# Optimization experiments

Measured on AMD Instinct MI355X. Metric: run time of the kernel, lower is better.

Reference implementation:

```python
import jax, jax.numpy as jnp
import numpy as np

NBR_SIZE = 3
ALPHA = -1.0
EPS = 1e-12  # torch F.normalize eps


def _l2norm(x, axis):
    n = jnp.sqrt(jnp.sum(x * x, axis=axis, keepdims=True))
    return x / jnp.maximum(n, EPS)


def setup_inputs() -> dict:
    key = jax.random.key(0)
    k1, k2 = jax.random.split(key)
    nbrs = jax.random.normal(k1, (4, 4, 64, 128, 128), dtype=jnp.float32)  # [b, n_frames, c, h, w]
    ref = jax.random.normal(k2, (4, 64, 128, 128), dtype=jnp.float32)      # [b, c, h, w]
    return {"nbrs": nbrs, "ref": ref}


def reference(nbrs, ref):
    b, n, c, h, w = nbrs.shape
    pad = NBR_SIZE // 2
    # mean over neighbor frames, detached in the original
    mean = jax.lax.stop_gradient(jnp.mean(nbrs, axis=1))          # [b,c,h,w]
    # ref is detached+cloned before normalization in the original
    ref_n = _l2norm(jax.lax.stop_gradient(ref), axis=1)           # [b,c,h,w], unit-norm over c

    outs = []
    for i in range(n):  # small fixed number of frames
        nbr = nbrs[:, i]                                          # [b,c,h,w]
        wdiff = jnp.exp(ALPHA * (nbr - mean) ** 2)                # [b,c,h,w]
        p = jnp.pad(nbr, ((0, 0), (0, 0), (pad, pad), (pad, pad)), mode='reflect')
        # unfold: k2 = NBR_SIZE**2 shifted views -> [b,c,k2,h,w]
        win = jnp.stack([p[:, :, dy:dy + h, dx:dx + w]
                         for dy in range(NBR_SIZE) for dx in range(NBR_SIZE)], axis=2)
        win_n = _l2norm(win, axis=1)                              # normalize over channels
        # per-pixel cosine similarity: [b,k2,h,w]
        d = jnp.einsum('bchw,bckhw->bkhw', ref_n, win_n)
        wt = jax.nn.softmax(d, axis=1)                            # softmax over k2 window positions
        # aggregate normalized window features: [b,c,h,w]
        agg = jnp.einsum('bkhw,bckhw->bchw', wt, win_n)
        outs.append(agg * wdiff)

    return jnp.stack(outs + [ref], axis=1)                        # [b, n+1, c, h, w]
```

## Files before the change

kernel.cpp:

```cpp
#include <hip/hip_runtime.h>
#include <math.h>

namespace {

constexpr int B_ = 4, N_ = 4, C_ = 64, H_ = 128, W_ = 128;
constexpr int HW_ = H_ * W_;
constexpr int CPB = 4;
constexpr int NWIN = C_ / CPB;

__global__ __launch_bounds__(256) void copyref_kernel(const float* __restrict__ ref,
                                                      float* __restrict__ out) {
    int t = blockIdx.x * 256 + threadIdx.x;
    int f = t * 4;
    int b = f / (C_ * HW_);
    int within = f - b * (C_ * HW_);
    float4 v = *reinterpret_cast<const float4*>(ref + (size_t)b * C_ * HW_ + within);
    *reinterpret_cast<float4*>(out + (size_t)(b * 5 + N_) * C_ * HW_ + within) = v;
}

__global__ __launch_bounds__(256) void localcorr_kernel(const float* __restrict__ nbrs,
                                                        const float* __restrict__ ref,
                                                        float* __restrict__ out) {
    __shared__ float s_own[2 * CPB][4][128];
    __shared__ float s_nrm[4][128];

    const int blk = blockIdx.x;
    const int ypair = blk & 63;
    const int bi = blk >> 6;
    const int i = bi & 3;
    const int b = bi >> 2;
    const int t = (int)threadIdx.x;
    const int x = t & 127;
    const int ry = t >> 7;
    const int y0 = ypair * 2;
    const int y = y0 + ry;

    const int xm = (x == 0) ? 1 : x - 1;
    const int xp = (x == W_ - 1) ? W_ - 2 : x + 1;
    const int gyA = (y0 == 0) ? 1 : y0 - 1;
    const int gyC = y0 + 1;
    const int gyD = (y0 + 2 == H_) ? H_ - 2 : y0 + 2;
    const int myRowA = (ry == 0) ? gyA : gyC;
    const int myRowB = (ry == 0) ? y0 : gyD;

    const float* __restrict__ nb = nbrs + (size_t)(b * N_ + i) * C_ * HW_;
    const float* __restrict__ rp = ref + (size_t)b * C_ * HW_;
    const int offA = myRowA * W_ + x;
    const int offB = myRowB * W_ + x;
    const int offR = y * W_ + x;

    float dot[9];
#pragma unroll
    for (int k = 0; k < 9; ++k) dot[k] = 0.f;
    float nA = 0.f, nB = 0.f, r2 = 0.f;

    float co0[CPB], co1[CPB], crf[CPB];
    float no0[CPB], no1[CPB], nrf[CPB];
#pragma unroll
    for (int u = 0; u < CPB; ++u) {
        const size_t co = (size_t)u * HW_;
        co0[u] = nb[co + offA]; co1[u] = nb[co + offB]; crf[u] = rp[co + offR];
    }
#pragma unroll 1
    for (int w = 0; w < NWIN; ++w) {
        const int base = (w & 1) * CPB;
#pragma unroll
        for (int u = 0; u < CPB; ++u) {
            s_own[base + u][2 * ry + 0][x] = co0[u];
            s_own[base + u][2 * ry + 1][x] = co1[u];
        }
        __syncthreads();
        if (w + 1 < NWIN) {
#pragma unroll
            for (int u = 0; u < CPB; ++u) {
                const size_t co = (size_t)((w + 1) * CPB + u) * HW_;
                no0[u] = nb[co + offA]; no1[u] = nb[co + offB]; nrf[u] = rp[co + offR];
            }
        }
#pragma unroll
        for (int u = 0; u < CPB; ++u) {
            const float w00 = s_own[base + u][ry + 0][xm], w02 = s_own[base + u][ry + 0][xp];
            const float w10 = s_own[base + u][ry + 1][xm], w12 = s_own[base + u][ry + 1][xp];
            const float w20 = s_own[base + u][ry + 2][xm], w22 = s_own[base + u][ry + 2][xp];
            float w01, w11, w21;
            if (ry == 0) { w01 = co0[u]; w11 = co1[u]; w21 = s_own[base + u][2][x]; }
            else         { w01 = s_own[base + u][1][x]; w11 = co0[u]; w21 = co1[u]; }
            const float rf = crf[u];
            nA += co0[u] * co0[u]; nB += co1[u] * co1[u]; r2 += rf * rf;
            dot[0] += rf * w00; dot[1] += rf * w01; dot[2] += rf * w02;
            dot[3] += rf * w10; dot[4] += rf * w11; dot[5] += rf * w12;
            dot[6] += rf * w20; dot[7] += rf * w21; dot[8] += rf * w22;
        }
#pragma unroll
        for (int u = 0; u < CPB; ++u) { co0[u] = no0[u]; co1[u] = no1[u]; crf[u] = nrf[u]; }
    }

    s_nrm[2 * ry + 0][x] = nA;
    s_nrm[2 * ry + 1][x] = nB;
    __syncthreads();
    float nk[9];
    nk[0] = s_nrm[ry + 0][xm]; nk[1] = s_nrm[ry + 0][x]; nk[2] = s_nrm[ry + 0][xp];
    nk[3] = s_nrm[ry + 1][xm]; nk[4] = s_nrm[ry + 1][x]; nk[5] = s_nrm[ry + 1][xp];
    nk[6] = s_nrm[ry + 2][xm]; nk[7] = s_nrm[ry + 2][x]; nk[8] = s_nrm[ry + 2][xp];

    const float invr = rsqrtf(fmaxf(r2, 1e-24f));
    float inv[9], d[9];
#pragma unroll
    for (int k = 0; k < 9; ++k) {
        inv[k] = rsqrtf(fmaxf(nk[k], 1e-24f));
        d[k] = dot[k] * invr * inv[k];
    }
    float mx = d[0];
#pragma unroll
    for (int k = 1; k < 9; ++k) mx = fmaxf(mx, d[k]);
    float ssum = 0.f;
#pragma unroll
    for (int k = 0; k < 9; ++k) { d[k] = __expf(d[k] - mx); ssum += d[k]; }
    const float is = 1.f / ssum;
    float wtp[9];
#pragma unroll
    for (int k = 0; k < 9; ++k) wtp[k] = d[k] * is * inv[k];

    const float* __restrict__ pm0 = nbrs + (size_t)(b * N_ + ((i + 1) & 3)) * C_ * HW_;
    const float* __restrict__ pm1 = nbrs + (size_t)(b * N_ + ((i + 2) & 3)) * C_ * HW_;
    const float* __restrict__ pm2 = nbrs + (size_t)(b * N_ + ((i + 3) & 3)) * C_ * HW_;
    float* __restrict__ op = out + (size_t)(b * 5 + i) * C_ * HW_ + offR;

    float q0c[CPB], q1c[CPB], q2c[CPB];
    float q0n[CPB], q1n[CPB], q2n[CPB];
#pragma unroll
    for (int u = 0; u < CPB; ++u) {
        const size_t co = (size_t)u * HW_;
        co0[u] = nb[co + offA]; co1[u] = nb[co + offB];
        q0c[u] = pm0[co + offR]; q1c[u] = pm1[co + offR]; q2c[u] = pm2[co + offR];
    }
#pragma unroll 1
    for (int w = 0; w < NWIN; ++w) {
        const int base = (w & 1) * CPB;
#pragma unroll
        for (int u = 0; u < CPB; ++u) {
            s_own[base + u][2 * ry + 0][x] = co0[u];
            s_own[base + u][2 * ry + 1][x] = co1[u];
        }
        __syncthreads();
        if (w + 1 < NWIN) {
#pragma unroll
            for (int u = 0; u < CPB; ++u) {
                const size_t co = (size_t)((w + 1) * CPB + u) * HW_;
                no0[u] = nb[co + offA]; no1[u] = nb[co + offB];
                q0n[u] = pm0[co + offR]; q1n[u] = pm1[co + offR]; q2n[u] = pm2[co + offR];
            }
        }
#pragma unroll
        for (int u = 0; u < CPB; ++u) {
            const float w00 = s_own[base + u][ry + 0][xm], w02 = s_own[base + u][ry + 0][xp];
            const float w10 = s_own[base + u][ry + 1][xm], w12 = s_own[base + u][ry + 1][xp];
            const float w20 = s_own[base + u][ry + 2][xm], w22 = s_own[base + u][ry + 2][xp];
            float w01, w11, w21;
            if (ry == 0) { w01 = co0[u]; w11 = co1[u]; w21 = s_own[base + u][2][x]; }
            else         { w01 = s_own[base + u][1][x]; w11 = co0[u]; w21 = co1[u]; }
            const float agg = wtp[0] * w00 + wtp[1] * w01 + wtp[2] * w02
                            + wtp[3] * w10 + wtp[4] * w11 + wtp[5] * w12
                            + wtp[6] * w20 + wtp[7] * w21 + wtp[8] * w22;
            const float ctr = w11;
            const float dd = ctr - 0.25f * (ctr + q0c[u] + q1c[u] + q2c[u]);
            op[(size_t)(w * CPB + u) * HW_] = agg * __expf(-dd * dd);
        }
#pragma unroll
        for (int u = 0; u < CPB; ++u) {
            co0[u] = no0[u]; co1[u] = no1[u];
            q0c[u] = q0n[u]; q1c[u] = q1n[u]; q2c[u] = q2n[u];
        }
    }
}

}

extern "C" void kernel_launch(void* const* d_in, const int* in_sizes, int n_in,
                              void* d_out, int out_size, void* d_ws, size_t ws_size,
                              hipStream_t stream) {
    const float* nbrs = (const float*)d_in[0];
    const float* ref = (const float*)d_in[1];
    float* out = (float*)d_out;

    copyref_kernel<<<(B_ * C_ * HW_ / 4) / 256, 256, 0, stream>>>(ref, out);

    localcorr_kernel<<<B_ * N_ * (H_ / 2), 256, 0, stream>>>(nbrs, ref, out);
}
```

Before: 74.84 us.

## Tile four rows per block with two pixels per thread and float2 loads

Each block now covers 4 output rows instead of 2, and each thread handles two adjacent x pixels using float2 loads and stores. Halo rows are loaded by the first 128 threads and stored in a 6-row shared buffer. This cuts halo re-reads of neighbour rows from 2x to 1.5x and halves the number of memory instructions. In exchange the grid shrinks to 512 blocks, some threads sit idle during halo loads, and register pressure goes up from the two 9-element accumulator sets.

After: 67.31 us. 10.1% less time.

```diff
diff --git a/kernel.cpp b/kernel.cpp
--- a/kernel.cpp
+++ b/kernel.cpp
@@ -7,6 +7,7 @@
 constexpr int HW_ = H_ * W_;
 constexpr int CPB = 4;
 constexpr int NWIN = C_ / CPB;
+constexpr int ROWS = 4;
 
 __global__ __launch_bounds__(256) void copyref_kernel(const float* __restrict__ ref,
                                                       float* __restrict__ out) {
@@ -18,157 +19,212 @@
     *reinterpret_cast<float4*>(out + (size_t)(b * 5 + N_) * C_ * HW_ + within) = v;
 }
 
+__device__ __forceinline__ float2 ld2(const float* p) {
+    return *reinterpret_cast<const float2*>(p);
+}
+
 __global__ __launch_bounds__(256) void localcorr_kernel(const float* __restrict__ nbrs,
                                                         const float* __restrict__ ref,
                                                         float* __restrict__ out) {
-    __shared__ float s_own[2 * CPB][4][128];
-    __shared__ float s_nrm[4][128];
+    __shared__ float2 s_own[2 * CPB][6][64];
+    __shared__ float2 s_nrm[6][64];
 
     const int blk = blockIdx.x;
-    const int ypair = blk & 63;
-    const int bi = blk >> 6;
+    const int ytile = blk & 31;
+    const int bi = blk >> 5;
     const int i = bi & 3;
     const int b = bi >> 2;
     const int t = (int)threadIdx.x;
-    const int x = t & 127;
-    const int ry = t >> 7;
-    const int y0 = ypair * 2;
+    const int xh = t & 63;
+    const int ry = t >> 6;
+    const int x0 = xh * 2;
+    const int y0 = ytile * ROWS;
     const int y = y0 + ry;
 
-    const int xm = (x == 0) ? 1 : x - 1;
-    const int xp = (x == W_ - 1) ? W_ - 2 : x + 1;
-    const int gyA = (y0 == 0) ? 1 : y0 - 1;
-    const int gyC = y0 + 1;
-    const int gyD = (y0 + 2 == H_) ? H_ - 2 : y0 + 2;
-    const int myRowA = (ry == 0) ? gyA : gyC;
-    const int myRowB = (ry == 0) ? y0 : gyD;
+    const int xlh = (xh == 0) ? 0 : xh - 1;
+    const int xrh = (xh == 63) ? 63 : xh + 1;
+    const int gTop = (y0 == 0) ? 1 : y0 - 1;
+    const int gBot = (y0 + ROWS == H_) ? H_ - 2 : y0 + ROWS;
+
+    const bool isHalo = (t < 128);
+    const int haloRow = (t < 64) ? 0 : 5;
+    const int haloOff = ((t < 64) ? gTop : gBot) * W_ + x0;
 
     const float* __restrict__ nb = nbrs + (size_t)(b * N_ + i) * C_ * HW_;
     const float* __restrict__ rp = ref + (size_t)b * C_ * HW_;
-    const int offA = myRowA * W_ + x;
-    const int offB = myRowB * W_ + x;
-    const int offR = y * W_ + x;
-
-    float dot[9];
-#pragma unroll
-    for (int k = 0; k < 9; ++k) dot[k] = 0.f;
-    float nA = 0.f, nB = 0.f, r2 = 0.f;
-
-    float co0[CPB], co1[CPB], crf[CPB];
-    float no0[CPB], no1[CPB], nrf[CPB];
+    const int offO = y * W_ + x0;
+
+    float d0[9], d1[9];
+#pragma unroll
+    for (int k = 0; k < 9; ++k) { d0[k] = 0.f; d1[k] = 0.f; }
+    float na = 0.f, nb2 = 0.f, r20 = 0.f, r21 = 0.f, hna = 0.f, hnb = 0.f;
+
+    float2 cO[CPB], cR[CPB], cH[CPB];
+    float2 nO[CPB], nR[CPB], nH[CPB];
 #pragma unroll
     for (int u = 0; u < CPB; ++u) {
         const size_t co = (size_t)u * HW_;
-        co0[u] = nb[co + offA]; co1[u] = nb[co + offB]; crf[u] = rp[co + offR];
+        cO[u] = ld2(nb + co + offO);
+        cR[u] = ld2(rp + co + offO);
+        cH[u] = isHalo ? ld2(nb + co + haloOff) : make_float2(0.f, 0.f);
+        nH[u] = make_float2(0.f, 0.f);
     }
 #pragma unroll 1
     for (int w = 0; w < NWIN; ++w) {
         const int base = (w & 1) * CPB;
 #pragma unroll
         for (int u = 0; u < CPB; ++u) {
-            s_own[base + u][2 * ry + 0][x] = co0[u];
-            s_own[base + u][2 * ry + 1][x] = co1[u];
+            s_own[base + u][ry + 1][xh] = cO[u];
+            if (isHalo) s_own[base + u][haloRow][xh] = cH[u];
         }
         __syncthreads();
         if (w + 1 < NWIN) {
 #pragma unroll
             for (int u = 0; u < CPB; ++u) {
                 const size_t co = (size_t)((w + 1) * CPB + u) * HW_;
-                no0[u] = nb[co + offA]; no1[u] = nb[co + offB]; nrf[u] = rp[co + offR];
-            }
-        }
-#pragma unroll
-        for (int u = 0; u < CPB; ++u) {
-            const float w00 = s_own[base + u][ry + 0][xm], w02 = s_own[base + u][ry + 0][xp];
-            const float w10 = s_own[base + u][ry + 1][xm], w12 = s_own[base + u][ry + 1][xp];
-            const float w20 = s_own[base + u][ry + 2][xm], w22 = s_own[base + u][ry + 2][xp];
-            float w01, w11, w21;
-            if (ry == 0) { w01 = co0[u]; w11 = co1[u]; w21 = s_own[base + u][2][x]; }
-            else         { w01 = s_own[base + u][1][x]; w11 = co0[u]; w21 = co1[u]; }
-            const float rf = crf[u];
-            nA += co0[u] * co0[u]; nB += co1[u] * co1[u]; r2 += rf * rf;
-            dot[0] += rf * w00; dot[1] += rf * w01; dot[2] += rf * w02;
-            dot[3] += rf * w10; dot[4] += rf * w11; dot[5] += rf * w12;
-            dot[6] += rf * w20; dot[7] += rf * w21; dot[8] += rf * w22;
-        }
-#pragma unroll
-        for (int u = 0; u < CPB; ++u) { co0[u] = no0[u]; co1[u] = no1[u]; crf[u] = nrf[u]; }
-    }
-
-    s_nrm[2 * ry + 0][x] = nA;
-    s_nrm[2 * ry + 1][x] = nB;
+                nO[u] = ld2(nb + co + offO);
+                nR[u] = ld2(rp + co + offO);
+                if (isHalo) nH[u] = ld2(nb + co + haloOff);
+            }
+        }
+#pragma unroll
+        for (int u = 0; u < CPB; ++u) {
+            const float2 rf = cR[u];
+            r20 += rf.x * rf.x; r21 += rf.y * rf.y;
+            na += cO[u].x * cO[u].x; nb2 += cO[u].y * cO[u].y;
+            if (isHalo) { hna += cH[u].x * cH[u].x; hnb += cH[u].y * cH[u].y; }
+#pragma unroll
+            for (int wr = 0; wr < 3; ++wr) {
+                const int r = ry + wr;
+                const float2 Lp = s_own[base + u][r][xlh];
+                const float2 Cp = (wr == 1) ? cO[u] : s_own[base + u][r][xh];
+                const float2 Rp = s_own[base + u][r][xrh];
+                d0[3 * wr + 0] += rf.x * Lp.y;
+                d0[3 * wr + 1] += rf.x * Cp.x;
+                d0[3 * wr + 2] += rf.x * Cp.y;
+                d1[3 * wr + 0] += rf.y * Cp.x;
+                d1[3 * wr + 1] += rf.y * Cp.y;
+                d1[3 * wr + 2] += rf.y * Rp.x;
+            }
+        }
+#pragma unroll
+        for (int u = 0; u < CPB; ++u) { cO[u] = nO[u]; cR[u] = nR[u]; cH[u] = nH[u]; }
+    }
+
+    s_nrm[ry + 1][xh] = make_float2(na, nb2);
+    if (isHalo) s_nrm[haloRow][xh] = make_float2(hna, hnb);
     __syncthreads();
-    float nk[9];
-    nk[0] = s_nrm[ry + 0][xm]; nk[1] = s_nrm[ry + 0][x]; nk[2] = s_nrm[ry + 0][xp];
-    nk[3] = s_nrm[ry + 1][xm]; nk[4] = s_nrm[ry + 1][x]; nk[5] = s_nrm[ry + 1][xp];
-    nk[6] = s_nrm[ry + 2][xm]; nk[7] = s_nrm[ry + 2][x]; nk[8] = s_nrm[ry + 2][xp];
-
-    const float invr = rsqrtf(fmaxf(r2, 1e-24f));
-    float inv[9], d[9];
-#pragma unroll
-    for (int k = 0; k < 9; ++k) {
-        inv[k] = rsqrtf(fmaxf(nk[k], 1e-24f));
-        d[k] = dot[k] * invr * inv[k];
-    }
-    float mx = d[0];
-#pragma unroll
-    for (int k = 1; k < 9; ++k) mx = fmaxf(mx, d[k]);
-    float ssum = 0.f;
-#pragma unroll
-    for (int k = 0; k < 9; ++k) { d[k] = __expf(d[k] - mx); ssum += d[k]; }
-    const float is = 1.f / ssum;
-    float wtp[9];
-#pragma unroll
-    for (int k = 0; k < 9; ++k) wtp[k] = d[k] * is * inv[k];
+
+    float nk0[9], nk1[9];
+#pragma unroll
+    for (int wr = 0; wr < 3; ++wr) {
+        const int r = ry + wr;
+        const float2 Lp = s_nrm[r][xlh];
+        const float2 Cp = (wr == 1) ? make_float2(na, nb2) : s_nrm[r][xh];
+        const float2 Rp = s_nrm[r][xrh];
+        nk0[3 * wr + 0] = Lp.y; nk0[3 * wr + 1] = Cp.x; nk0[3 * wr + 2] = Cp.y;
+        nk1[3 * wr + 0] = Cp.x; nk1[3 * wr + 1] = Cp.y; nk1[3 * wr + 2] = Rp.x;
+    }
+
+    float w0[9], w1[9];
+    {
+        const float invr = rsqrtf(fmaxf(r20, 1e-24f));
+        float iv[9], dd[9];
+#pragma unroll
+        for (int k = 0; k < 9; ++k) {
+            iv[k] = rsqrtf(fmaxf(nk0[k], 1e-24f));
+            dd[k] = d0[k] * invr * iv[k];
+        }
+        float mx = dd[0];
+#pragma unroll
+        for (int k = 1; k < 9; ++k) mx = fmaxf(mx, dd[k]);
+        float ss = 0.f;
+#pragma unroll
+        for (int k = 0; k < 9; ++k) { dd[k] = __expf(dd[k] - mx); ss += dd[k]; }
+        const float is = 1.f / ss;
+#pragma unroll
+        for (int k = 0; k < 9; ++k) w0[k] = dd[k] * is * iv[k];
+    }
+    {
+        const float invr = rsqrtf(fmaxf(r21, 1e-24f));
+        float iv[9], dd[9];
+#pragma unroll
+        for (int k = 0; k < 9; ++k) {
+            iv[k] = rsqrtf(fmaxf(nk1[k], 1e-24f));
+            dd[k] = d1[k] * invr * iv[k];
+        }
+        float mx = dd[0];
+#pragma unroll
+        for (int k = 1; k < 9; ++k) mx = fmaxf(mx, dd[k]);
+        float ss = 0.f;
+#pragma unroll
+        for (int k = 0; k < 9; ++k) { dd[k] = __expf(dd[k] - mx); ss += dd[k]; }
+        const float is = 1.f / ss;
+#pragma unroll
+        for (int k = 0; k < 9; ++k) w1[k] = dd[k] * is * iv[k];
+    }
 
     const float* __restrict__ pm0 = nbrs + (size_t)(b * N_ + ((i + 1) & 3)) * C_ * HW_;
     const float* __restrict__ pm1 = nbrs + (size_t)(b * N_ + ((i + 2) & 3)) * C_ * HW_;
     const float* __restrict__ pm2 = nbrs + (size_t)(b * N_ + ((i + 3) & 3)) * C_ * HW_;
-    float* __restrict__ op = out + (size_t)(b * 5 + i) * C_ * HW_ + offR;
-
-    float q0c[CPB], q1c[CPB], q2c[CPB];
-    float q0n[CPB], q1n[CPB], q2n[CPB];
+    float* __restrict__ op = out + (size_t)(b * 5 + i) * C_ * HW_ + offO;
+
+    float2 q0c[CPB], q1c[CPB], q2c[CPB];
+    float2 q0n[CPB], q1n[CPB], q2n[CPB];
 #pragma unroll
     for (int u = 0; u < CPB; ++u) {
         const size_t co = (size_t)u * HW_;
-        co0[u] = nb[co + offA]; co1[u] = nb[co + offB];
-        q0c[u] = pm0[co + offR]; q1c[u] = pm1[co + offR]; q2c[u] = pm2[co + offR];
+        cO[u] = ld2(nb + co + offO);
+        cH[u] = isHalo ? ld2(nb + co + haloOff) : make_float2(0.f, 0.f);
+        q0c[u] = ld2(pm0 + co + offO);
+        q1c[u] = ld2(pm1 + co + offO);
+        q2c[u] = ld2(pm2 + co + offO);
     }
 #pragma unroll 1
     for (int w = 0; w < NWIN; ++w) {
         const int base = (w & 1) * CPB;
 #pragma unroll
         for (int u = 0; u < CPB; ++u) {
-            s_own[base + u][2 * ry + 0][x] = co0[u];
-            s_own[base + u][2 * ry + 1][x] = co1[u];
+            s_own[base + u][ry + 1][xh] = cO[u];
+            if (isHalo) s_own[base + u][haloRow][xh] = cH[u];
         }
         __syncthreads();
         if (w + 1 < NWIN) {
 #pragma unroll
             for (int u = 0; u < CPB; ++u) {
                 const size_t co = (size_t)((w + 1) * CPB + u) * HW_;
-                no0[u] = nb[co + offA]; no1[u] = nb[co + offB];
-                q0n[u] = pm0[co + offR]; q1n[u] = pm1[co + offR]; q2n[u] = pm2[co + offR];
-            }
-        }
-#pragma unroll
-        for (int u = 0; u < CPB; ++u) {
-            const float w00 = s_own[base + u][ry + 0][xm], w02 = s_own[base + u][ry + 0][xp];
-            const float w10 = s_own[base + u][ry + 1][xm], w12 = s_own[base + u][ry + 1][xp];
-            const float w20 = s_own[base + u][ry + 2][xm], w22 = s_own[base + u][ry + 2][xp];
-            float w01, w11, w21;
-            if (ry == 0) { w01 = co0[u]; w11 = co1[u]; w21 = s_own[base + u][2][x]; }
-            else         { w01 = s_own[base + u][1][x]; w11 = co0[u]; w21 = co1[u]; }
-            const float agg = wtp[0] * w00 + wtp[1] * w01 + wtp[2] * w02
-                            + wtp[3] * w10 + wtp[4] * w11 + wtp[5] * w12
-                            + wtp[6] * w20 + wtp[7] * w21 + wtp[8] * w22;
-            const float ctr = w11;
-            const float dd = ctr - 0.25f * (ctr + q0c[u] + q1c[u] + q2c[u]);
-            op[(size_t)(w * CPB + u) * HW_] = agg * __expf(-dd * dd);
-        }
-#pragma unroll
-        for (int u = 0; u < CPB; ++u) {
-            co0[u] = no0[u]; co1[u] = no1[u];
+                nO[u] = ld2(nb + co + offO);
+                if (isHalo) nH[u] = ld2(nb + co + haloOff);
+                q0n[u] = ld2(pm0 + co + offO);
+                q1n[u] = ld2(pm1 + co + offO);
+                q2n[u] = ld2(pm2 + co + offO);
+            }
+        }
+#pragma unroll
+        for (int u = 0; u < CPB; ++u) {
+            float agg0 = 0.f, agg1 = 0.f;
+#pragma unroll
+            for (int wr = 0; wr < 3; ++wr) {
+                const int r = ry + wr;
+                const float2 Lp = s_own[base + u][r][xlh];
+                const float2 Cp = (wr == 1) ? cO[u] : s_own[base + u][r][xh];
+                const float2 Rp = s_own[base + u][r][xrh];
+                agg0 += w0[3 * wr + 0] * Lp.y + w0[3 * wr + 1] * Cp.x + w0[3 * wr + 2] * Cp.y;
+                agg1 += w1[3 * wr + 0] * Cp.x + w1[3 * wr + 1] * Cp.y + w1[3 * wr + 2] * Rp.x;
+            }
+            const float2 ctr = cO[u];
+            const float s0 = ctr.x + q0c[u].x + q1c[u].x + q2c[u].x;
+            const float s1 = ctr.y + q0c[u].y + q1c[u].y + q2c[u].y;
+            const float dd0 = ctr.x - 0.25f * s0;
+            const float dd1 = ctr.y - 0.25f * s1;
+            float2 o2;
+            o2.x = agg0 * __expf(-dd0 * dd0);
+            o2.y = agg1 * __expf(-dd1 * dd1);
+            *reinterpret_cast<float2*>(op + (size_t)(w * CPB + u) * HW_) = o2;
+        }
+#pragma unroll
+        for (int u = 0; u < CPB; ++u) {
+            cO[u] = nO[u]; cH[u] = nH[u];
             q0c[u] = q0n[u]; q1c[u] = q1n[u]; q2c[u] = q2n[u];
         }
     }
@@ -185,5 +241,5 @@
 
     copyref_kernel<<<(B_ * C_ * HW_ / 4) / 256, 256, 0, stream>>>(ref, out);
 
-    localcorr_kernel<<<B_ * N_ * (H_ / 2), 256, 0, stream>>>(nbrs, ref, out);
-}
+    localcorr_kernel<<<B_ * N_ * (H_ / ROWS), 256, 0, stream>>>(nbrs, ref, out);
+}
```

## Process all four neighbor frames per block to share ref and mean loads

Applied to the files above, without the earlier changes.

Each block now handles one (batch, row-pair) tile for all four frames instead of one frame, so the grid shrinks from 1024 to 256 blocks. The reference channel values are loaded once and reused across frames. The frame mean comes from the center values already in registers, so the three extra neighbor-frame loads in the second pass go away. In exchange, register and shared-memory use per thread grow sharply, and with only one block per CU there is much less parallelism to hide memory latency.

After: 165.7 us. +121.5%, slower.

```diff
diff --git a/kernel.cpp b/kernel.cpp
--- a/kernel.cpp
+++ b/kernel.cpp
@@ -21,14 +21,12 @@
 __global__ __launch_bounds__(256) void localcorr_kernel(const float* __restrict__ nbrs,
                                                         const float* __restrict__ ref,
                                                         float* __restrict__ out) {
-    __shared__ float s_own[2 * CPB][4][128];
-    __shared__ float s_nrm[4][128];
+    __shared__ float s_win[2][CPB][4][4][128];
+    __shared__ float s_nrm[4][4][128];
 
     const int blk = blockIdx.x;
     const int ypair = blk & 63;
-    const int bi = blk >> 6;
-    const int i = bi & 3;
-    const int b = bi >> 2;
+    const int b = blk >> 6;
     const int t = (int)threadIdx.x;
     const int x = t & 127;
     const int ry = t >> 7;
@@ -43,134 +41,183 @@
     const int myRowA = (ry == 0) ? gyA : gyC;
     const int myRowB = (ry == 0) ? y0 : gyD;
 
-    const float* __restrict__ nb = nbrs + (size_t)(b * N_ + i) * C_ * HW_;
+    const float* __restrict__ nbq[4];
+#pragma unroll
+    for (int j = 0; j < 4; ++j) nbq[j] = nbrs + (size_t)(b * N_ + j) * C_ * HW_;
     const float* __restrict__ rp = ref + (size_t)b * C_ * HW_;
     const int offA = myRowA * W_ + x;
     const int offB = myRowB * W_ + x;
     const int offR = y * W_ + x;
 
-    float dot[9];
-#pragma unroll
-    for (int k = 0; k < 9; ++k) dot[k] = 0.f;
-    float nA = 0.f, nB = 0.f, r2 = 0.f;
-
-    float co0[CPB], co1[CPB], crf[CPB];
-    float no0[CPB], no1[CPB], nrf[CPB];
+    float dot[4][9];
+#pragma unroll
+    for (int j = 0; j < 4; ++j)
+#pragma unroll
+        for (int k = 0; k < 9; ++k) dot[j][k] = 0.f;
+    float nA[4], nB[4];
+#pragma unroll
+    for (int j = 0; j < 4; ++j) { nA[j] = 0.f; nB[j] = 0.f; }
+    float r2 = 0.f;
+
+    float c0[CPB][4], c1[CPB][4], crf[CPB];
+    float n0[CPB][4], n1[CPB][4], nrf[CPB];
 #pragma unroll
     for (int u = 0; u < CPB; ++u) {
         const size_t co = (size_t)u * HW_;
-        co0[u] = nb[co + offA]; co1[u] = nb[co + offB]; crf[u] = rp[co + offR];
+#pragma unroll
+        for (int j = 0; j < 4; ++j) {
+            c0[u][j] = nbq[j][co + offA];
+            c1[u][j] = nbq[j][co + offB];
+        }
+        crf[u] = rp[co + offR];
     }
 #pragma unroll 1
     for (int w = 0; w < NWIN; ++w) {
-        const int base = (w & 1) * CPB;
-#pragma unroll
-        for (int u = 0; u < CPB; ++u) {
-            s_own[base + u][2 * ry + 0][x] = co0[u];
-            s_own[base + u][2 * ry + 1][x] = co1[u];
-        }
+        const int buf = w & 1;
+#pragma unroll
+        for (int u = 0; u < CPB; ++u)
+#pragma unroll
+            for (int j = 0; j < 4; ++j) {
+                s_win[buf][u][j][2 * ry + 0][x] = c0[u][j];
+                s_win[buf][u][j][2 * ry + 1][x] = c1[u][j];
+            }
         __syncthreads();
         if (w + 1 < NWIN) {
 #pragma unroll
             for (int u = 0; u < CPB; ++u) {
                 const size_t co = (size_t)((w + 1) * CPB + u) * HW_;
-                no0[u] = nb[co + offA]; no1[u] = nb[co + offB]; nrf[u] = rp[co + offR];
+#pragma unroll
+                for (int j = 0; j < 4; ++j) {
+                    n0[u][j] = nbq[j][co + offA];
+                    n1[u][j] = nbq[j][co + offB];
+                }
+                nrf[u] = rp[co + offR];
             }
         }
 #pragma unroll
         for (int u = 0; u < CPB; ++u) {
-            const float w00 = s_own[base + u][ry + 0][xm], w02 = s_own[base + u][ry + 0][xp];
-            const float w10 = s_own[base + u][ry + 1][xm], w12 = s_own[base + u][ry + 1][xp];
-            const float w20 = s_own[base + u][ry + 2][xm], w22 = s_own[base + u][ry + 2][xp];
-            float w01, w11, w21;
-            if (ry == 0) { w01 = co0[u]; w11 = co1[u]; w21 = s_own[base + u][2][x]; }
-            else         { w01 = s_own[base + u][1][x]; w11 = co0[u]; w21 = co1[u]; }
             const float rf = crf[u];
-            nA += co0[u] * co0[u]; nB += co1[u] * co1[u]; r2 += rf * rf;
-            dot[0] += rf * w00; dot[1] += rf * w01; dot[2] += rf * w02;
-            dot[3] += rf * w10; dot[4] += rf * w11; dot[5] += rf * w12;
-            dot[6] += rf * w20; dot[7] += rf * w21; dot[8] += rf * w22;
-        }
-#pragma unroll
-        for (int u = 0; u < CPB; ++u) { co0[u] = no0[u]; co1[u] = no1[u]; crf[u] = nrf[u]; }
-    }
-
-    s_nrm[2 * ry + 0][x] = nA;
-    s_nrm[2 * ry + 1][x] = nB;
+            r2 += rf * rf;
+#pragma unroll
+            for (int j = 0; j < 4; ++j) {
+                const float* sc = &s_win[buf][u][j][0][0];
+                const float w00 = sc[(ry + 0) * 128 + xm], w02 = sc[(ry + 0) * 128 + xp];
+                const float w10 = sc[(ry + 1) * 128 + xm], w12 = sc[(ry + 1) * 128 + xp];
+                const float w20 = sc[(ry + 2) * 128 + xm], w22 = sc[(ry + 2) * 128 + xp];
+                float w01, w11, w21;
+                if (ry == 0) { w01 = c0[u][j]; w11 = c1[u][j]; w21 = sc[2 * 128 + x]; }
+                else         { w01 = sc[1 * 128 + x]; w11 = c0[u][j]; w21 = c1[u][j]; }
+                nA[j] += c0[u][j] * c0[u][j];
+                nB[j] += c1[u][j] * c1[u][j];
+                dot[j][0] += rf * w00; dot[j][1] += rf * w01; dot[j][2] += rf * w02;
+                dot[j][3] += rf * w10; dot[j][4] += rf * w11; dot[j][5] += rf * w12;
+                dot[j][6] += rf * w20; dot[j][7] += rf * w21; dot[j][8] += rf * w22;
+            }
+        }
+#pragma unroll
+        for (int u = 0; u < CPB; ++u) {
+#pragma unroll
+            for (int j = 0; j < 4; ++j) { c0[u][j] = n0[u][j]; c1[u][j] = n1[u][j]; }
+            crf[u] = nrf[u];
+        }
+    }
+
+#pragma unroll
+    for (int j = 0; j < 4; ++j) {
+        s_nrm[j][2 * ry + 0][x] = nA[j];
+        s_nrm[j][2 * ry + 1][x] = nB[j];
+    }
     __syncthreads();
-    float nk[9];
-    nk[0] = s_nrm[ry + 0][xm]; nk[1] = s_nrm[ry + 0][x]; nk[2] = s_nrm[ry + 0][xp];
-    nk[3] = s_nrm[ry + 1][xm]; nk[4] = s_nrm[ry + 1][x]; nk[5] = s_nrm[ry + 1][xp];
-    nk[6] = s_nrm[ry + 2][xm]; nk[7] = s_nrm[ry + 2][x]; nk[8] = s_nrm[ry + 2][xp];
 
     const float invr = rsqrtf(fmaxf(r2, 1e-24f));
-    float inv[9], d[9];
-#pragma unroll
-    for (int k = 0; k < 9; ++k) {
-        inv[k] = rsqrtf(fmaxf(nk[k], 1e-24f));
-        d[k] = dot[k] * invr * inv[k];
-    }
-    float mx = d[0];
-#pragma unroll
-    for (int k = 1; k < 9; ++k) mx = fmaxf(mx, d[k]);
-    float ssum = 0.f;
-#pragma unroll
-    for (int k = 0; k < 9; ++k) { d[k] = __expf(d[k] - mx); ssum += d[k]; }
-    const float is = 1.f / ssum;
-    float wtp[9];
-#pragma unroll
-    for (int k = 0; k < 9; ++k) wtp[k] = d[k] * is * inv[k];
-
-    const float* __restrict__ pm0 = nbrs + (size_t)(b * N_ + ((i + 1) & 3)) * C_ * HW_;
-    const float* __restrict__ pm1 = nbrs + (size_t)(b * N_ + ((i + 2) & 3)) * C_ * HW_;
-    const float* __restrict__ pm2 = nbrs + (size_t)(b * N_ + ((i + 3) & 3)) * C_ * HW_;
-    float* __restrict__ op = out + (size_t)(b * 5 + i) * C_ * HW_ + offR;
-
-    float q0c[CPB], q1c[CPB], q2c[CPB];
-    float q0n[CPB], q1n[CPB], q2n[CPB];
+    float wtp[4][9];
+#pragma unroll
+    for (int j = 0; j < 4; ++j) {
+        float nk[9];
+        nk[0] = s_nrm[j][ry + 0][xm]; nk[1] = s_nrm[j][ry + 0][x]; nk[2] = s_nrm[j][ry + 0][xp];
+        nk[3] = s_nrm[j][ry + 1][xm]; nk[4] = s_nrm[j][ry + 1][x]; nk[5] = s_nrm[j][ry + 1][xp];
+        nk[6] = s_nrm[j][ry + 2][xm]; nk[7] = s_nrm[j][ry + 2][x]; nk[8] = s_nrm[j][ry + 2][xp];
+        float iv[9], d[9];
+#pragma unroll
+        for (int k = 0; k < 9; ++k) {
+            iv[k] = rsqrtf(fmaxf(nk[k], 1e-24f));
+            d[k] = dot[j][k] * invr * iv[k];
+        }
+        float mx = d[0];
+#pragma unroll
+        for (int k = 1; k < 9; ++k) mx = fmaxf(mx, d[k]);
+        float ss = 0.f;
+#pragma unroll
+        for (int k = 0; k < 9; ++k) { d[k] = __expf(d[k] - mx); ss += d[k]; }
+        const float is = 1.f / ss;
+#pragma unroll
+        for (int k = 0; k < 9; ++k) wtp[j][k] = d[k] * is * iv[k];
+    }
+
+    float* __restrict__ op[4];
+#pragma unroll
+    for (int j = 0; j < 4; ++j) op[j] = out + (size_t)(b * 5 + j) * C_ * HW_ + offR;
+
 #pragma unroll
     for (int u = 0; u < CPB; ++u) {
         const size_t co = (size_t)u * HW_;
-        co0[u] = nb[co + offA]; co1[u] = nb[co + offB];
-        q0c[u] = pm0[co + offR]; q1c[u] = pm1[co + offR]; q2c[u] = pm2[co + offR];
+#pragma unroll
+        for (int j = 0; j < 4; ++j) {
+            c0[u][j] = nbq[j][co + offA];
+            c1[u][j] = nbq[j][co + offB];
+        }
     }
 #pragma unroll 1
     for (int w = 0; w < NWIN; ++w) {
-        const int base = (w & 1) * CPB;
-#pragma unroll
-        for (int u = 0; u < CPB; ++u) {
-            s_own[base + u][2 * ry + 0][x] = co0[u];
-            s_own[base + u][2 * ry + 1][x] = co1[u];
-        }
+        const int buf = w & 1;
+#pragma unroll
+        for (int u = 0; u < CPB; ++u)
+#pragma unroll
+            for (int j = 0; j < 4; ++j) {
+                s_win[buf][u][j][2 * ry + 0][x] = c0[u][j];
+                s_win[buf][u][j][2 * ry + 1][x] = c1[u][j];
+            }
         __syncthreads();
         if (w + 1 < NWIN) {
 #pragma unroll
             for (int u = 0; u < CPB; ++u) {
                 const size_t co = (size_t)((w + 1) * CPB + u) * HW_;
-                no0[u] = nb[co + offA]; no1[u] = nb[co + offB];
-                q0n[u] = pm0[co + offR]; q1n[u] = pm1[co + offR]; q2n[u] = pm2[co + offR];
+#pragma unroll
+                for (int j = 0; j < 4; ++j) {
+                    n0[u][j] = nbq[j][co + offA];
+                    n1[u][j] = nbq[j][co + offB];
+                }
             }
         }
 #pragma unroll
         for (int u = 0; u < CPB; ++u) {
-            const float w00 = s_own[base + u][ry + 0][xm], w02 = s_own[base + u][ry + 0][xp];
-            const float w10 = s_own[base + u][ry + 1][xm], w12 = s_own[base + u][ry + 1][xp];
-            const float w20 = s_own[base + u][ry + 2][xm], w22 = s_own[base + u][ry + 2][xp];
-            float w01, w11, w21;
-            if (ry == 0) { w01 = co0[u]; w11 = co1[u]; w21 = s_own[base + u][2][x]; }
-            else         { w01 = s_own[base + u][1][x]; w11 = co0[u]; w21 = co1[u]; }
-            const float agg = wtp[0] * w00 + wtp[1] * w01 + wtp[2] * w02
-                            + wtp[3] * w10 + wtp[4] * w11 + wtp[5] * w12
-                            + wtp[6] * w20 + wtp[7] * w21 + wtp[8] * w22;
-            const float ctr = w11;
-            const float dd = ctr - 0.25f * (ctr + q0c[u] + q1c[u] + q2c[u]);
-            op[(size_t)(w * CPB + u) * HW_] = agg * __expf(-dd * dd);
-        }
-#pragma unroll
-        for (int u = 0; u < CPB; ++u) {
-            co0[u] = no0[u]; co1[u] = no1[u];
-            q0c[u] = q0n[u]; q1c[u] = q1n[u]; q2c[u] = q2n[u];
-        }
+            float agg[4], ctr[4];
+#pragma unroll
+            for (int j = 0; j < 4; ++j) {
+                const float* sc = &s_win[buf][u][j][0][0];
+                const float w00 = sc[(ry + 0) * 128 + xm], w02 = sc[(ry + 0) * 128 + xp];
+                const float w10 = sc[(ry + 1) * 128 + xm], w12 = sc[(ry + 1) * 128 + xp];
+                const float w20 = sc[(ry + 2) * 128 + xm], w22 = sc[(ry + 2) * 128 + xp];
+                float w01, w11, w21;
+                if (ry == 0) { w01 = c0[u][j]; w11 = c1[u][j]; w21 = sc[2 * 128 + x]; }
+                else         { w01 = sc[1 * 128 + x]; w11 = c0[u][j]; w21 = c1[u][j]; }
+                agg[j] = wtp[j][0] * w00 + wtp[j][1] * w01 + wtp[j][2] * w02
+                       + wtp[j][3] * w10 + wtp[j][4] * w11 + wtp[j][5] * w12
+                       + wtp[j][6] * w20 + wtp[j][7] * w21 + wtp[j][8] * w22;
+                ctr[j] = w11;
+            }
+            const float mu = 0.25f * (ctr[0] + ctr[1] + ctr[2] + ctr[3]);
+            const size_t co = (size_t)(w * CPB + u) * HW_;
+#pragma unroll
+            for (int j = 0; j < 4; ++j) {
+                const float dd = ctr[j] - mu;
+                op[j][co] = agg[j] * __expf(-dd * dd);
+            }
+        }
+#pragma unroll
+        for (int u = 0; u < CPB; ++u)
+#pragma unroll
+            for (int j = 0; j < 4; ++j) { c0[u][j] = n0[u][j]; c1[u][j] = n1[u][j]; }
     }
 }
 
@@ -185,5 +232,5 @@
 
     copyref_kernel<<<(B_ * C_ * HW_ / 4) / 256, 256, 0, stream>>>(ref, out);
 
-    localcorr_kernel<<<B_ * N_ * (H_ / 2), 256, 0, stream>>>(nbrs, ref, out);
-}
+    localcorr_kernel<<<B_ * (H_ / 2), 256, 0, stream>>>(nbrs, ref, out);
+}
```

## Split channel reduction across two thread groups with shared-memory combine

Applied to the files above, without the earlier changes.

Doubles the block to 512 threads, with each half handling 32 of the 64 channels for the same pixels. Partial dot products, ref norms and window norms are combined through shared memory before the softmax. The global prefetch is also moved ahead of the barrier so loads overlap the sync. This halves the serial channel-loop length per thread to raise parallelism and latency hiding, at the cost of extra barriers, a reduction step, and more shared memory per block.

Result: slower. 80.57 us (+7.7%).

```diff
diff --git a/kernel.cpp b/kernel.cpp
--- a/kernel.cpp
+++ b/kernel.cpp
@@ -6,7 +6,8 @@
 constexpr int B_ = 4, N_ = 4, C_ = 64, H_ = 128, W_ = 128;
 constexpr int HW_ = H_ * W_;
 constexpr int CPB = 4;
-constexpr int NWIN = C_ / CPB;
+constexpr int CHQ = 32;
+constexpr int NWIN = CHQ / CPB;
 
 __global__ __launch_bounds__(256) void copyref_kernel(const float* __restrict__ ref,
                                                       float* __restrict__ out) {
@@ -18,10 +19,10 @@
     *reinterpret_cast<float4*>(out + (size_t)(b * 5 + N_) * C_ * HW_ + within) = v;
 }
 
-__global__ __launch_bounds__(256) void localcorr_kernel(const float* __restrict__ nbrs,
+__global__ __launch_bounds__(512) void localcorr_kernel(const float* __restrict__ nbrs,
                                                         const float* __restrict__ ref,
                                                         float* __restrict__ out) {
-    __shared__ float s_own[2 * CPB][4][128];
+    __shared__ float s_mem[8192];
     __shared__ float s_nrm[4][128];
 
     const int blk = blockIdx.x;
@@ -31,9 +32,12 @@
     const int b = bi >> 2;
     const int t = (int)threadIdx.x;
     const int x = t & 127;
-    const int ry = t >> 7;
+    const int ry = (t >> 7) & 1;
+    const int q = t >> 8;
+    const int px = t & 255;
     const int y0 = ypair * 2;
     const int y = y0 + ry;
+    const int cb = q * CHQ;
 
     const int xm = (x == 0) ? 1 : x - 1;
     const int xp = (x == W_ - 1) ? W_ - 2 : x + 1;
@@ -58,33 +62,34 @@
     float no0[CPB], no1[CPB], nrf[CPB];
 #pragma unroll
     for (int u = 0; u < CPB; ++u) {
-        const size_t co = (size_t)u * HW_;
+        const size_t co = (size_t)(cb + u) * HW_;
         co0[u] = nb[co + offA]; co1[u] = nb[co + offB]; crf[u] = rp[co + offR];
     }
 #pragma unroll 1
     for (int w = 0; w < NWIN; ++w) {
-        const int base = (w & 1) * CPB;
-#pragma unroll
-        for (int u = 0; u < CPB; ++u) {
-            s_own[base + u][2 * ry + 0][x] = co0[u];
-            s_own[base + u][2 * ry + 1][x] = co1[u];
-        }
-        __syncthreads();
+        float* wb = s_mem + q * 4096 + (w & 1) * 2048;
+#pragma unroll
+        for (int u = 0; u < CPB; ++u) {
+            wb[u * 512 + (2 * ry + 0) * 128 + x] = co0[u];
+            wb[u * 512 + (2 * ry + 1) * 128 + x] = co1[u];
+        }
         if (w + 1 < NWIN) {
 #pragma unroll
             for (int u = 0; u < CPB; ++u) {
-                const size_t co = (size_t)((w + 1) * CPB + u) * HW_;
+                const size_t co = (size_t)(cb + (w + 1) * CPB + u) * HW_;
                 no0[u] = nb[co + offA]; no1[u] = nb[co + offB]; nrf[u] = rp[co + offR];
             }
         }
-#pragma unroll
-        for (int u = 0; u < CPB; ++u) {
-            const float w00 = s_own[base + u][ry + 0][xm], w02 = s_own[base + u][ry + 0][xp];
-            const float w10 = s_own[base + u][ry + 1][xm], w12 = s_own[base + u][ry + 1][xp];
-            const float w20 = s_own[base + u][ry + 2][xm], w22 = s_own[base + u][ry + 2][xp];
+        __syncthreads();
+#pragma unroll
+        for (int u = 0; u < CPB; ++u) {
+            const float* sc = wb + u * 512;
+            const float w00 = sc[(ry + 0) * 128 + xm], w02 = sc[(ry + 0) * 128 + xp];
+            const float w10 = sc[(ry + 1) * 128 + xm], w12 = sc[(ry + 1) * 128 + xp];
+            const float w20 = sc[(ry + 2) * 128 + xm], w22 = sc[(ry + 2) * 128 + xp];
             float w01, w11, w21;
-            if (ry == 0) { w01 = co0[u]; w11 = co1[u]; w21 = s_own[base + u][2][x]; }
-            else         { w01 = s_own[base + u][1][x]; w11 = co0[u]; w21 = co1[u]; }
+            if (ry == 0) { w01 = co0[u]; w11 = co1[u]; w21 = sc[2 * 128 + x]; }
+            else         { w01 = sc[1 * 128 + x]; w11 = co0[u]; w21 = co1[u]; }
             const float rf = crf[u];
             nA += co0[u] * co0[u]; nB += co1[u] * co1[u]; r2 += rf * rf;
             dot[0] += rf * w00; dot[1] += rf * w01; dot[2] += rf * w02;
@@ -95,9 +100,25 @@
         for (int u = 0; u < CPB; ++u) { co0[u] = no0[u]; co1[u] = no1[u]; crf[u] = nrf[u]; }
     }
 
-    s_nrm[2 * ry + 0][x] = nA;
-    s_nrm[2 * ry + 1][x] = nB;
-    __syncthreads();
+    __syncthreads();
+#pragma unroll
+    for (int k = 0; k < 9; ++k) s_mem[q * 2304 + k * 256 + px] = dot[k];
+    s_mem[4608 + q * 256 + px] = r2;
+    if (q == 0) {
+        s_nrm[2 * ry + 0][x] = nA;
+        s_nrm[2 * ry + 1][x] = nB;
+    }
+    __syncthreads();
+    if (q == 1) {
+        s_nrm[2 * ry + 0][x] += nA;
+        s_nrm[2 * ry + 1][x] += nB;
+    }
+    const int oq = 1 - q;
+#pragma unroll
+    for (int k = 0; k < 9; ++k) dot[k] += s_mem[oq * 2304 + k * 256 + px];
+    r2 += s_mem[4608 + oq * 256 + px];
+    __syncthreads();
+
     float nk[9];
     nk[0] = s_nrm[ry + 0][xm]; nk[1] = s_nrm[ry + 0][x]; nk[2] = s_nrm[ry + 0][xp];
     nk[3] = s_nrm[ry + 1][xm]; nk[4] = s_nrm[ry + 1][x]; nk[5] = s_nrm[ry + 1][xp];
@@ -121,6 +142,8 @@
 #pragma unroll
     for (int k = 0; k < 9; ++k) wtp[k] = d[k] * is * inv[k];
 
+    __syncthreads();
+
     const float* __restrict__ pm0 = nbrs + (size_t)(b * N_ + ((i + 1) & 3)) * C_ * HW_;
     const float* __restrict__ pm1 = nbrs + (size_t)(b * N_ + ((i + 2) & 3)) * C_ * HW_;
     const float* __restrict__ pm2 = nbrs + (size_t)(b * N_ + ((i + 3) & 3)) * C_ * HW_;
@@ -130,41 +153,42 @@
     float q0n[CPB], q1n[CPB], q2n[CPB];
 #pragma unroll
     for (int u = 0; u < CPB; ++u) {
-        const size_t co = (size_t)u * HW_;
+        const size_t co = (size_t)(cb + u) * HW_;
         co0[u] = nb[co + offA]; co1[u] = nb[co + offB];
         q0c[u] = pm0[co + offR]; q1c[u] = pm1[co + offR]; q2c[u] = pm2[co + offR];
     }
 #pragma unroll 1
     for (int w = 0; w < NWIN; ++w) {
-        const int base = (w & 1) * CPB;
-#pragma unroll
-        for (int u = 0; u < CPB; ++u) {
-            s_own[base + u][2 * ry + 0][x] = co0[u];
-            s_own[base + u][2 * ry + 1][x] = co1[u];
-        }
-        __syncthreads();
+        float* wb = s_mem + q * 4096 + (w & 1) * 2048;
+#pragma unroll
+        for (int u = 0; u < CPB; ++u) {
+            wb[u * 512 + (2 * ry + 0) * 128 + x] = co0[u];
+            wb[u * 512 + (2 * ry + 1) * 128 + x] = co1[u];
+        }
         if (w + 1 < NWIN) {
 #pragma unroll
             for (int u = 0; u < CPB; ++u) {
-                const size_t co = (size_t)((w + 1) * CPB + u) * HW_;
+                const size_t co = (size_t)(cb + (w + 1) * CPB + u) * HW_;
                 no0[u] = nb[co + offA]; no1[u] = nb[co + offB];
                 q0n[u] = pm0[co + offR]; q1n[u] = pm1[co + offR]; q2n[u] = pm2[co + offR];
             }
         }
-#pragma unroll
-        for (int u = 0; u < CPB; ++u) {
-            const float w00 = s_own[base + u][ry + 0][xm], w02 = s_own[base + u][ry + 0][xp];
-            const float w10 = s_own[base + u][ry + 1][xm], w12 = s_own[base + u][ry + 1][xp];
-            const float w20 = s_own[base + u][ry + 2][xm], w22 = s_own[base + u][ry + 2][xp];
+        __syncthreads();
+#pragma unroll
+        for (int u = 0; u < CPB; ++u) {
+            const float* sc = wb + u * 512;
+            const float w00 = sc[(ry + 0) * 128 + xm], w02 = sc[(ry + 0) * 128 + xp];
+            const float w10 = sc[(ry + 1) * 128 + xm], w12 = sc[(ry + 1) * 128 + xp];
+            const float w20 = sc[(ry + 2) * 128 + xm], w22 = sc[(ry + 2) * 128 + xp];
             float w01, w11, w21;
-            if (ry == 0) { w01 = co0[u]; w11 = co1[u]; w21 = s_own[base + u][2][x]; }
-            else         { w01 = s_own[base + u][1][x]; w11 = co0[u]; w21 = co1[u]; }
+            if (ry == 0) { w01 = co0[u]; w11 = co1[u]; w21 = sc[2 * 128 + x]; }
+            else         { w01 = sc[1 * 128 + x]; w11 = co0[u]; w21 = co1[u]; }
             const float agg = wtp[0] * w00 + wtp[1] * w01 + wtp[2] * w02
                             + wtp[3] * w10 + wtp[4] * w11 + wtp[5] * w12
                             + wtp[6] * w20 + wtp[7] * w21 + wtp[8] * w22;
             const float ctr = w11;
             const float dd = ctr - 0.25f * (ctr + q0c[u] + q1c[u] + q2c[u]);
-            op[(size_t)(w * CPB + u) * HW_] = agg * __expf(-dd * dd);
+            op[(size_t)(cb + w * CPB + u) * HW_] = agg * __expf(-dd * dd);
         }
 #pragma unroll
         for (int u = 0; u < CPB; ++u) {
@@ -185,5 +209,5 @@
 
     copyref_kernel<<<(B_ * C_ * HW_ / 4) / 256, 256, 0, stream>>>(ref, out);
 
-    localcorr_kernel<<<B_ * N_ * (H_ / 2), 256, 0, stream>>>(nbrs, ref, out);
-}
+    localcorr_kernel<<<B_ * N_ * (H_ / 2), 512, 0, stream>>>(nbrs, ref, out);
+}
```
